# Performance work log

Hardware: AMD Instinct MI355X
Metric: run time of the kernel (lower is better)

## Reference

```python
import jax, jax.numpy as jnp
import numpy as np

N = 100000
E = 1600000
F_IN = 64
HID = 64
N_CLS = 10


def setup_inputs() -> dict:
    key = jax.random.key(0)
    ks = jax.random.split(key, 16)
    x = jax.random.normal(ks[0], (N, F_IN), dtype=jnp.float32)
    edge_index = jax.random.randint(ks[1], (2, E), 0, N, dtype=jnp.int64)

    def lin(k, fin, fout):
        s = 1.0 / np.sqrt(fin)
        return jax.random.uniform(k, (fin, fout), jnp.float32, -s, s)

    inp = {"x": x, "edge_index": edge_index}
    # SAGEConv params: lin_l (neighbors, with bias), lin_r (root, no bias)
    dims = [(F_IN, HID), (HID, HID), (HID, HID)]
    for i, (fin, fout) in enumerate(dims, start=1):
        inp[f"Wl{i}"] = lin(ks[3 * i - 1], fin, fout)
        inp[f"bl{i}"] = jnp.zeros((fout,), jnp.float32)
        inp[f"Wr{i}"] = lin(ks[3 * i], fin, fout)
    inp["Wc"] = lin(ks[12], HID, N_CLS)
    inp["bc"] = jnp.zeros((N_CLS,), jnp.float32)
    return inp


def _sage(x, src, dst, Wl, bl, Wr):
    # mean aggregation of neighbor messages x[src] at dst nodes
    n = x.shape[0]
    agg = jax.ops.segment_sum(x[src], dst, num_segments=n)  # [N, F]
    cnt = jax.ops.segment_sum(jnp.ones((src.shape[0],), x.dtype), dst, num_segments=n)
    mean = agg / jnp.maximum(cnt, 1.0)[:, None]
    return mean @ Wl + bl + x @ Wr


def reference(x, edge_index, Wl1, bl1, Wr1, Wl2, bl2, Wr2, Wl3, bl3, Wr3, Wc, bc):
    src, dst = edge_index[0], edge_index[1]
    h = jax.nn.relu(_sage(x, src, dst, Wl1, bl1, Wr1))  # dropout = identity (eval)
    h = jax.nn.relu(_sage(h, src, dst, Wl2, bl2, Wr2))
    h = jax.nn.relu(_sage(h, src, dst, Wl3, bl3, Wr3))
    out = h @ Wc + bc
    return jax.nn.log_softmax(out, axis=1)
```

## Files before the change

### kernel.cpp

```cpp
#include <hip/hip_runtime.h>
#include <hip/hip_bf16.h>
#include <math.h>


#define BSHIFT 8
#define BUCKET 256
#define MAXB 512
#define SCAT_EDGES 8192
#define TROWS 128

__global__ __launch_bounds__(256) void hist_kernel(const int* __restrict__ dst,
                                                   int* __restrict__ ghist,
                                                   int E, int nbuck) {
    __shared__ int lh[MAXB];
    int t = threadIdx.x;
    lh[t] = 0; lh[t + 256] = 0;
    __syncthreads();
    int start = blockIdx.x * SCAT_EDGES;
    int end = min(E, start + SCAT_EDGES);
    for (int e = start + t; e < end; e += 256)
        atomicAdd(&lh[dst[e] >> BSHIFT], 1);
    __syncthreads();
    for (int b = t; b < nbuck; b += 256)
        if (lh[b]) atomicAdd(&ghist[b], lh[b]);
}

__global__ __launch_bounds__(512) void scanb_kernel(const int* __restrict__ ghist,
                                                    int* __restrict__ bbase,
                                                    int* __restrict__ gcur,
                                                    int nbuck, int E) {
    __shared__ int s[MAXB];
    int t = threadIdx.x;
    int v = (t < nbuck) ? ghist[t] : 0;
    s[t] = v;
    __syncthreads();
    for (int off = 1; off < MAXB; off <<= 1) {
        int u = (t >= off) ? s[t - off] : 0;
        __syncthreads();
        s[t] += u;
        __syncthreads();
    }
    int excl = s[t] - v;
    if (t < nbuck) { bbase[t] = excl; gcur[t] = excl; }
    if (t == 0) bbase[nbuck] = E;
}

__global__ __launch_bounds__(256) void scatter_kernel(const int* __restrict__ src,
                                                      const int* __restrict__ dst,
                                                      int* __restrict__ gcur,
                                                      unsigned int* __restrict__ pairs,
                                                      int E, int nbuck) {
    __shared__ int lh[MAXB];
    __shared__ int lbase[MAXB];
    __shared__ int lcur[MAXB];
    int t = threadIdx.x;
    lh[t] = 0; lh[t + 256] = 0;
    lcur[t] = 0; lcur[t + 256] = 0;
    __syncthreads();
    int start = blockIdx.x * SCAT_EDGES;
    int end = min(E, start + SCAT_EDGES);
    for (int e = start + t; e < end; e += 256)
        atomicAdd(&lh[dst[e] >> BSHIFT], 1);
    __syncthreads();
    for (int b = t; b < nbuck; b += 256)
        if (lh[b]) lbase[b] = atomicAdd(&gcur[b], lh[b]);
    __syncthreads();
    for (int e = start + t; e < end; e += 256) {
        int d = dst[e];
        int b = d >> BSHIFT;
        int slot = atomicAdd(&lcur[b], 1);
        pairs[lbase[b] + slot] = ((unsigned int)src[e] << BSHIFT) | (unsigned int)(d & (BUCKET - 1));
    }
}

__global__ __launch_bounds__(256) void build_kernel(const unsigned int* __restrict__ pairs,
                                                    const int* __restrict__ bbase,
                                                    int* __restrict__ rowptr,
                                                    int* __restrict__ col,
                                                    int n, int E) {
    __shared__ int ldeg[BUCKET];
    __shared__ int pre[BUCKET];
    __shared__ int cur[BUCKET];
    int t = threadIdx.x;
    int nbase = blockIdx.x << BSHIFT;
    int e0 = bbase[blockIdx.x], e1 = bbase[blockIdx.x + 1];
    ldeg[t] = 0; cur[t] = 0;
    __syncthreads();
    for (int e = e0 + t; e < e1; e += 256)
        atomicAdd(&ldeg[pairs[e] & (BUCKET - 1)], 1);
    __syncthreads();
    int v = ldeg[t];
    pre[t] = v;
    __syncthreads();
    for (int off = 1; off < 256; off <<= 1) {
        int u = (t >= off) ? pre[t - off] : 0;
        __syncthreads();
        pre[t] += u;
        __syncthreads();
    }
    int excl = pre[t] - v;
    __syncthreads();
    pre[t] = excl;
    __syncthreads();
    int node = nbase + t;
    if (node < n) rowptr[node] = e0 + excl;
    if (blockIdx.x == 0 && t == 0) rowptr[n] = E;
    for (int e = e0 + t; e < e1; e += 256) {
        unsigned int p = pairs[e];
        int l = (int)(p & (BUCKET - 1));
        int pos = atomicAdd(&cur[l], 1);
        col[e0 + pre[l] + pos] = (int)(p >> BSHIFT);
    }
}

__global__ __launch_bounds__(256, 4) void transform_kernel(
    const float* in, float* Qh, __hip_bfloat16* __restrict__ Pb,
    const float* __restrict__ Wl, const float* __restrict__ bl,
    const float* __restrict__ Wr, int n)
{
    __shared__ float4 tile[TROWS * 16];
    int tid = threadIdx.x;
    int c = tid & 127;
    int grp = tid >> 7;
    bool isQ = (c >= 64);
    int f = c & 63;
    const float* W = isQ ? Wr : Wl;
    float bias = isQ ? bl[f] : 0.f;

    int base = blockIdx.x * TROWS;
    int nvalid = n - base; if (nvalid > TROWS) nvalid = TROWS;
    const float4* srcp = (const float4*)(in + (size_t)base * 64);
    for (int i = tid; i < nvalid * 16; i += 256) tile[i] = srcp[i];
    __syncthreads();

    #pragma unroll 1
    for (int s = 0; s < 4; ++s) {
        int r0 = (grp << 6) + (s << 4);
        if (r0 >= nvalid) continue;
        float a[16];
        #pragma unroll
        for (int i = 0; i < 16; ++i) a[i] = bias;
        #pragma unroll 1
        for (int kq = 0; kq < 16; ++kq) {
            float w0 = W[(4 * kq + 0) * 64 + f];
            float w1 = W[(4 * kq + 1) * 64 + f];
            float w2 = W[(4 * kq + 2) * 64 + f];
            float w3 = W[(4 * kq + 3) * 64 + f];
            #pragma unroll
            for (int rc = 0; rc < 4; ++rc) {
                float4 x0 = tile[(r0 + rc * 4 + 0) * 16 + kq];
                float4 x1 = tile[(r0 + rc * 4 + 1) * 16 + kq];
                float4 x2 = tile[(r0 + rc * 4 + 2) * 16 + kq];
                float4 x3 = tile[(r0 + rc * 4 + 3) * 16 + kq];
                a[rc * 4 + 0] = fmaf(x0.w, w3, fmaf(x0.z, w2, fmaf(x0.y, w1, fmaf(x0.x, w0, a[rc * 4 + 0]))));
                a[rc * 4 + 1] = fmaf(x1.w, w3, fmaf(x1.z, w2, fmaf(x1.y, w1, fmaf(x1.x, w0, a[rc * 4 + 1]))));
                a[rc * 4 + 2] = fmaf(x2.w, w3, fmaf(x2.z, w2, fmaf(x2.y, w1, fmaf(x2.x, w0, a[rc * 4 + 2]))));
                a[rc * 4 + 3] = fmaf(x3.w, w3, fmaf(x3.z, w2, fmaf(x3.y, w1, fmaf(x3.x, w0, a[rc * 4 + 3]))));
            }
        }
        #pragma unroll
        for (int i = 0; i < 16; ++i) {
            int v = base + r0 + i;
            if (v < n) {
                if (isQ) Qh[(size_t)v * 64 + f] = a[i];
                else     Pb[(size_t)v * 64 + f] = __float2bfloat16(a[i]);
            }
        }
    }
}

__global__ __launch_bounds__(256) void gather_kernel(
    const __hip_bfloat16* __restrict__ Pb, float* __restrict__ Qh,
    const int* __restrict__ rowptr, const int* __restrict__ col, int n)
{
    int tid = threadIdx.x;
    int wid = tid >> 6, lane = tid & 63;
    int w = blockIdx.x * 4 + wid;
    int nw = gridDim.x * 4;
    for (int v = w; v < n; v += nw) {
        int s0 = rowptr[v], s1 = rowptr[v + 1];
        int deg = s1 - s0;
        float q = Qh[(size_t)v * 64 + lane];
        float acc = 0.f;
        for (int base = 0; base < deg; base += 64) {
            int rem = deg - base;
            int cnt = rem < 64 ? rem : 64;
            int ci = (lane < cnt) ? col[s0 + base + lane] : 0;
            int j = 0;
            for (; j + 8 <= cnt; j += 8) {
                int i0 = __shfl(ci, j + 0), i1 = __shfl(ci, j + 1);
                int i2 = __shfl(ci, j + 2), i3 = __shfl(ci, j + 3);
                int i4 = __shfl(ci, j + 4), i5 = __shfl(ci, j + 5);
                int i6 = __shfl(ci, j + 6), i7 = __shfl(ci, j + 7);
                float t0 = __bfloat162float(Pb[(size_t)i0 * 64 + lane]);
                float t1 = __bfloat162float(Pb[(size_t)i1 * 64 + lane]);
                float t2 = __bfloat162float(Pb[(size_t)i2 * 64 + lane]);
                float t3 = __bfloat162float(Pb[(size_t)i3 * 64 + lane]);
                float t4 = __bfloat162float(Pb[(size_t)i4 * 64 + lane]);
                float t5 = __bfloat162float(Pb[(size_t)i5 * 64 + lane]);
                float t6 = __bfloat162float(Pb[(size_t)i6 * 64 + lane]);
                float t7 = __bfloat162float(Pb[(size_t)i7 * 64 + lane]);
                acc += ((t0 + t1) + (t2 + t3)) + ((t4 + t5) + (t6 + t7));
            }
            for (; j + 4 <= cnt; j += 4) {
                int i0 = __shfl(ci, j + 0), i1 = __shfl(ci, j + 1);
                int i2 = __shfl(ci, j + 2), i3 = __shfl(ci, j + 3);
                float t0 = __bfloat162float(Pb[(size_t)i0 * 64 + lane]);
                float t1 = __bfloat162float(Pb[(size_t)i1 * 64 + lane]);
                float t2 = __bfloat162float(Pb[(size_t)i2 * 64 + lane]);
                float t3 = __bfloat162float(Pb[(size_t)i3 * 64 + lane]);
                acc += (t0 + t1) + (t2 + t3);
            }
            for (; j < cnt; ++j)
                acc += __bfloat162float(Pb[(size_t)__shfl(ci, j) * 64 + lane]);
        }
        float res = acc / fmaxf((float)deg, 1.0f) + q;
        Qh[(size_t)v * 64 + lane] = fmaxf(res, 0.f);
    }
}

__global__ __launch_bounds__(256) void cls_kernel(
    const float* __restrict__ h, const float* __restrict__ Wc,
    const float* __restrict__ bc, float* __restrict__ out, int n)
{
    __shared__ float sW[64 * 10];
    __shared__ float sb[16];
    __shared__ float srow[4][4][64];
    int tid = threadIdx.x;
    for (int i = tid; i < 640; i += 256) sW[i] = Wc[i];
    if (tid < 10) sb[tid] = bc[tid];
    __syncthreads();

    int wid = tid >> 6, lane = tid & 63;
    int grp = lane >> 4, l16 = lane & 15;
    int w = blockIdx.x * 4 + wid;
    int nw = gridDim.x * 4;
    int ngroups = (n + 3) >> 2;
    for (int g = w; g < ngroups; g += nw) {
        int v0 = g * 4;
        #pragma unroll
        for (int r = 0; r < 4; ++r) {
            int vv = v0 + r;
            if (vv < n) srow[wid][r][lane] = h[(size_t)vv * 64 + lane];
        }
        int v = v0 + grp;
        float z = -INFINITY;
        if (v < n && l16 < 10) {
            z = sb[l16];
            #pragma unroll
            for (int k = 0; k < 64; ++k)
                z += srow[wid][grp][k] * sW[k * 10 + l16];
        }
        float m = z;
        for (int off = 8; off > 0; off >>= 1)
            m = fmaxf(m, __shfl_xor(m, off, 16));
        float e = (l16 < 10 && v < n) ? expf(z - m) : 0.f;
        float ssum = e;
        for (int off = 8; off > 0; off >>= 1)
            ssum += __shfl_xor(ssum, off, 16);
        if (v < n && l16 < 10)
            out[(size_t)v * 10 + l16] = z - m - logf(ssum);
    }
}

extern "C" void kernel_launch(void* const* d_in, const int* in_sizes, int n_in,
                              void* d_out, int out_size, void* d_ws, size_t ws_size,
                              hipStream_t stream) {
    const float* x   = (const float*)d_in[0];
    const int*   ei  = (const int*)d_in[1];
    const float* Wl1 = (const float*)d_in[2];
    const float* bl1 = (const float*)d_in[3];
    const float* Wr1 = (const float*)d_in[4];
    const float* Wl2 = (const float*)d_in[5];
    const float* bl2 = (const float*)d_in[6];
    const float* Wr2 = (const float*)d_in[7];
    const float* Wl3 = (const float*)d_in[8];
    const float* bl3 = (const float*)d_in[9];
    const float* Wr3 = (const float*)d_in[10];
    const float* Wc  = (const float*)d_in[11];
    const float* bc  = (const float*)d_in[12];
    float* outp = (float*)d_out;

    int n = in_sizes[0] / 64;
    int E = in_sizes[1] / 2;
    const int* srcp = ei;
    const int* dstp = ei + E;
    int nbuck = (n + BUCKET - 1) >> BSHIFT;
    int SB = (E + SCAT_EDGES - 1) / SCAT_EDGES;
    int ntile = (n + TROWS - 1) / TROWS;

    char* ws = (char*)d_ws;
    size_t off = 0;
    auto alloc = [&](size_t bytes) -> void* {
        void* p = ws + off;
        off += bytes;
        off = (off + 255) & ~(size_t)255;
        return p;
    };
    int*   ghist  = (int*)alloc((size_t)MAXB * 4);
    int*   bbase  = (int*)alloc((size_t)(MAXB + 1) * 4);
    int*   gcur   = (int*)alloc((size_t)MAXB * 4);
    int*   rowptr = (int*)alloc((size_t)(n + 1) * 4);
    unsigned int* pairs = (unsigned int*)alloc((size_t)E * 4);
    int*   colv   = (int*)alloc((size_t)E * 4);
    __hip_bfloat16* Pb = (__hip_bfloat16*)alloc((size_t)n * 64 * 2);
    float* Qh     = (float*)alloc((size_t)n * 64 * 4);
    (void)ws_size; (void)n_in; (void)out_size;

    hipMemsetAsync(ghist, 0, (size_t)MAXB * 4, stream);

    hist_kernel<<<SB, 256, 0, stream>>>(dstp, ghist, E, nbuck);
    scanb_kernel<<<1, 512, 0, stream>>>(ghist, bbase, gcur, nbuck, E);
    scatter_kernel<<<SB, 256, 0, stream>>>(srcp, dstp, gcur, pairs, E, nbuck);
    build_kernel<<<nbuck, 256, 0, stream>>>(pairs, bbase, rowptr, colv, n, E);

    transform_kernel<<<ntile, 256, 0, stream>>>(x,  Qh, Pb, Wl1, bl1, Wr1, n);
    gather_kernel<<<2048, 256, 0, stream>>>(Pb, Qh, rowptr, colv, n);
    transform_kernel<<<ntile, 256, 0, stream>>>(Qh, Qh, Pb, Wl2, bl2, Wr2, n);
    gather_kernel<<<2048, 256, 0, stream>>>(Pb, Qh, rowptr, colv, n);
    transform_kernel<<<ntile, 256, 0, stream>>>(Qh, Qh, Pb, Wl3, bl3, Wr3, n);
    gather_kernel<<<2048, 256, 0, stream>>>(Pb, Qh, rowptr, colv, n);

    cls_kernel<<<1024, 256, 0, stream>>>(Qh, Wc, bc, outp, n);
}
```

Measured before the change: 439.9 us.

## Use 16x4 register tile per thread in transform kernel with vectorized stores

Restructures the dense transform so each thread computes a 16-row by 4-column output tile instead of 16 rows by one column. Weights are loaded as float4 and each LDS row read feeds four output columns, so there are fewer shared-memory and global weight loads per FMA. Outputs are written with float4 and packed 4-wide bf16 stores. Register use rises to 64 accumulators, so launch bounds drop from 4 to 3 waves, trading occupancy for more arithmetic per load.

```diff
diff --git a/kernel.cpp b/kernel.cpp
--- a/kernel.cpp
+++ b/kernel.cpp
@@ -113,57 +113,75 @@
     }
 }
 
-__global__ __launch_bounds__(256, 4) void transform_kernel(
+__global__ __launch_bounds__(256, 3) void transform_kernel(
     const float* in, float* Qh, __hip_bfloat16* __restrict__ Pb,
     const float* __restrict__ Wl, const float* __restrict__ bl,
     const float* __restrict__ Wr, int n)
 {
     __shared__ float4 tile[TROWS * 16];
     int tid = threadIdx.x;
-    int c = tid & 127;
-    int grp = tid >> 7;
-    bool isQ = (c >= 64);
-    int f = c & 63;
+    int tc = tid & 31;
+    int tr = tid >> 5;
+    bool isQ = (tc >= 16);
+    int f4 = (tc & 15) * 4;
     const float* W = isQ ? Wr : Wl;
-    float bias = isQ ? bl[f] : 0.f;
 
     int base = blockIdx.x * TROWS;
     int nvalid = n - base; if (nvalid > TROWS) nvalid = TROWS;
     const float4* srcp = (const float4*)(in + (size_t)base * 64);
     for (int i = tid; i < nvalid * 16; i += 256) tile[i] = srcp[i];
-    __syncthreads();
+
+    float b0 = 0.f, b1 = 0.f, b2 = 0.f, b3 = 0.f;
+    if (isQ) { b0 = bl[f4]; b1 = bl[f4 + 1]; b2 = bl[f4 + 2]; b3 = bl[f4 + 3]; }
+    __syncthreads();
+
+    float a[16][4];
+    #pragma unroll
+    for (int r = 0; r < 16; ++r) { a[r][0] = b0; a[r][1] = b1; a[r][2] = b2; a[r][3] = b3; }
 
     #pragma unroll 1
+    for (int kq = 0; kq < 16; ++kq) {
+        float4 w0 = *(const float4*)(W + (4 * kq + 0) * 64 + f4);
+        float4 w1 = *(const float4*)(W + (4 * kq + 1) * 64 + f4);
+        float4 w2 = *(const float4*)(W + (4 * kq + 2) * 64 + f4);
+        float4 w3 = *(const float4*)(W + (4 * kq + 3) * 64 + f4);
+        #pragma unroll
+        for (int s = 0; s < 4; ++s) {
+            #pragma unroll
+            for (int rr = 0; rr < 4; ++rr) {
+                int row = tr * 4 + s * 32 + rr;
+                float4 x = tile[row * 16 + kq];
+                int ai = s * 4 + rr;
+                a[ai][0] = fmaf(x.x, w0.x, a[ai][0]); a[ai][1] = fmaf(x.x, w0.y, a[ai][1]);
+                a[ai][2] = fmaf(x.x, w0.z, a[ai][2]); a[ai][3] = fmaf(x.x, w0.w, a[ai][3]);
+                a[ai][0] = fmaf(x.y, w1.x, a[ai][0]); a[ai][1] = fmaf(x.y, w1.y, a[ai][1]);
+                a[ai][2] = fmaf(x.y, w1.z, a[ai][2]); a[ai][3] = fmaf(x.y, w1.w, a[ai][3]);
+                a[ai][0] = fmaf(x.z, w2.x, a[ai][0]); a[ai][1] = fmaf(x.z, w2.y, a[ai][1]);
+                a[ai][2] = fmaf(x.z, w2.z, a[ai][2]); a[ai][3] = fmaf(x.z, w2.w, a[ai][3]);
+                a[ai][0] = fmaf(x.w, w3.x, a[ai][0]); a[ai][1] = fmaf(x.w, w3.y, a[ai][1]);
+                a[ai][2] = fmaf(x.w, w3.z, a[ai][2]); a[ai][3] = fmaf(x.w, w3.w, a[ai][3]);
+            }
+        }
+    }
+
+    #pragma unroll
     for (int s = 0; s < 4; ++s) {
-        int r0 = (grp << 6) + (s << 4);
-        if (r0 >= nvalid) continue;
-        float a[16];
         #pragma unroll
-        for (int i = 0; i < 16; ++i) a[i] = bias;
-        #pragma unroll 1
-        for (int kq = 0; kq < 16; ++kq) {
-            float w0 = W[(4 * kq + 0) * 64 + f];
-            float w1 = W[(4 * kq + 1) * 64 + f];
-            float w2 = W[(4 * kq + 2) * 64 + f];
-            float w3 = W[(4 * kq + 3) * 64 + f];
-            #pragma unroll
-            for (int rc = 0; rc < 4; ++rc) {
-                float4 x0 = tile[(r0 + rc * 4 + 0) * 16 + kq];
-                float4 x1 = tile[(r0 + rc * 4 + 1) * 16 + kq];
-                float4 x2 = tile[(r0 + rc * 4 + 2) * 16 + kq];
-                float4 x3 = tile[(r0 + rc * 4 + 3) * 16 + kq];
-                a[rc * 4 + 0] = fmaf(x0.w, w3, fmaf(x0.z, w2, fmaf(x0.y, w1, fmaf(x0.x, w0, a[rc * 4 + 0]))));
-                a[rc * 4 + 1] = fmaf(x1.w, w3, fmaf(x1.z, w2, fmaf(x1.y, w1, fmaf(x1.x, w0, a[rc * 4 + 1]))));
-                a[rc * 4 + 2] = fmaf(x2.w, w3, fmaf(x2.z, w2, fmaf(x2.y, w1, fmaf(x2.x, w0, a[rc * 4 + 2]))));
-                a[rc * 4 + 3] = fmaf(x3.w, w3, fmaf(x3.z, w2, fmaf(x3.y, w1, fmaf(x3.x, w0, a[rc * 4 + 3]))));
-            }
-        }
-        #pragma unroll
-        for (int i = 0; i < 16; ++i) {
-            int v = base + r0 + i;
-            if (v < n) {
-                if (isQ) Qh[(size_t)v * 64 + f] = a[i];
-                else     Pb[(size_t)v * 64 + f] = __float2bfloat16(a[i]);
+        for (int rr = 0; rr < 4; ++rr) {
+            int row = tr * 4 + s * 32 + rr;
+            int v = base + row;
+            if (v >= n) continue;
+            int ai = s * 4 + rr;
+            if (isQ) {
+                *(float4*)(Qh + (size_t)v * 64 + f4) =
+                    make_float4(a[ai][0], a[ai][1], a[ai][2], a[ai][3]);
+            } else {
+                union { ushort4 u4; __hip_bfloat16 b[4]; } pk;
+                pk.b[0] = __float2bfloat16(a[ai][0]);
+                pk.b[1] = __float2bfloat16(a[ai][1]);
+                pk.b[2] = __float2bfloat16(a[ai][2]);
+                pk.b[3] = __float2bfloat16(a[ai][3]);
+                *(ushort4*)((unsigned short*)Pb + (size_t)v * 64 + f4) = pk.u4;
             }
         }
     }
```

After: 384.3 us. 12.6% less time.
